# Performance work log

Hardware: AMD Instinct MI355X
Metric: run time of the kernel (lower is better)

## Reference

```python
import jax, jax.numpy as jnp
import numpy as np

B, T, C, H = 4, 2048, 768, 12
D = C // H  # head dim = 64

def setup_inputs() -> dict:
    key = jax.random.key(0)
    k1, k2, k3, k4, k5 = jax.random.split(key, 5)
    s = 0.02
    x = jax.random.normal(k1, (B, T, C), dtype=jnp.float32)
    w_qkv = jax.random.normal(k2, (3 * C, C), dtype=jnp.float32) * s  # torch Linear weight [out,in]
    b_qkv = jax.random.normal(k3, (3 * C,), dtype=jnp.float32) * s
    w_proj = jax.random.normal(k4, (C, C), dtype=jnp.float32) * s
    b_proj = jax.random.normal(k5, (C,), dtype=jnp.float32) * s
    return {"x": x, "w_qkv": w_qkv, "b_qkv": b_qkv, "w_proj": w_proj, "b_proj": b_proj}

def reference(x, w_qkv, b_qkv, w_proj, b_proj):
    Bx, Tx, Cx = x.shape
    # qkv projection: torch Linear y = x @ W.T + b
    qkv = x @ w_qkv.T + b_qkv                      # [B,T,3C]
    qkv = qkv.reshape(Bx, Tx, 3, H, D)
    q, k, v = qkv[:, :, 0], qkv[:, :, 1], qkv[:, :, 2]  # each [B,T,H,D]
    scale = 1.0 / jnp.sqrt(jnp.float32(D))
    scores = jnp.einsum('bqhd,bkhd->bhqk', q, k) * scale  # [B,H,T,T]
    causal = jnp.tril(jnp.ones((Tx, Tx), dtype=bool))
    scores = jnp.where(causal[None, None], scores, -jnp.inf)
    attn = jax.nn.softmax(scores, axis=-1)
    out = jnp.einsum('bhqk,bkhd->bqhd', attn, v).reshape(Bx, Tx, Cx)
    return out @ w_proj.T + b_proj
```

## Files before the change

kernel.cpp:

```cpp
#include <hip/hip_runtime.h>
#include <hip/hip_bf16.h>
#include <cstdint>
#include <cstddef>

typedef __bf16 bf16_t;
typedef __bf16 bf16x8 __attribute__((ext_vector_type(8)));
typedef __bf16 bf16x4 __attribute__((ext_vector_type(4)));
typedef float f32x4 __attribute__((ext_vector_type(4)));
typedef float f32x16 __attribute__((ext_vector_type(16)));

constexpr int B_ = 4, T_ = 2048, C_ = 768, H_ = 12, D_ = 64;
constexpr size_t QKV_ELEMS = (size_t)B_ * H_ * T_ * D_;
constexpr size_t AO_ELEMS  = (size_t)B_ * T_ * C_;
constexpr size_t WPB_ELEMS = (size_t)C_ * C_;

__device__ __forceinline__ void gload16(const bf16_t* g, bf16_t* l) {
    __builtin_amdgcn_global_load_lds(
        (const __attribute__((address_space(1))) unsigned int*)g,
        (__attribute__((address_space(3))) unsigned int*)l, 16, 0, 0);
}

__global__ __launch_bounds__(256)
void conv_bf16_3(const float* __restrict__ a, bf16_t* __restrict__ oa, int na8,
                 const float* __restrict__ b, bf16_t* __restrict__ ob, int nb8,
                 const float* __restrict__ c, bf16_t* __restrict__ oc, int nc8)
{
    int i = blockIdx.x * 256 + threadIdx.x;
    if (i >= na8 + nb8 + nc8) return;
    const float* src; bf16_t* dst; int idx;
    if (i < na8)             { src = a; dst = oa; idx = i; }
    else if (i < na8 + nb8)  { src = b; dst = ob; idx = i - na8; }
    else                     { src = c; dst = oc; idx = i - na8 - nb8; }
    const float4* p = reinterpret_cast<const float4*>(src + (size_t)idx * 8);
    float4 f0 = p[0], f1 = p[1];
    bf16x8 t;
    t[0]=(bf16_t)f0.x; t[1]=(bf16_t)f0.y; t[2]=(bf16_t)f0.z; t[3]=(bf16_t)f0.w;
    t[4]=(bf16_t)f1.x; t[5]=(bf16_t)f1.y; t[6]=(bf16_t)f1.z; t[7]=(bf16_t)f1.w;
    *reinterpret_cast<bf16x8*>(dst + (size_t)idx * 8) = t;
}

__global__ __launch_bounds__(256, 3)
void qkv_gemm(const bf16_t* __restrict__ xb, const bf16_t* __restrict__ wb,
              const float* __restrict__ bias,
              bf16_t* __restrict__ q, bf16_t* __restrict__ k, bf16_t* __restrict__ v)
{
    __shared__ alignas(16) bf16_t As[128 * 64];
    __shared__ alignas(16) bf16_t Bs[128 * 64];
    const int tid  = threadIdx.x;
    const int lane = tid & 63;
    const int w    = tid >> 6;
    const int wm = w >> 1, wn = w & 1;
    const int bm = blockIdx.x & 63;
    const int bn = blockIdx.x >> 6;
    const int m0 = bm * 128, n0 = bn * 128;
    const int lcol = lane & 15, lgrp = lane >> 4;
    const int srow = lane >> 3;
    const int scol = ((lane & 7) ^ srow) * 8;

    const bf16_t* ag = xb + (size_t)(m0 + w * 32 + srow) * C_ + scol;
    const bf16_t* bg = wb + (size_t)(n0 + w * 32 + srow) * C_ + scol;
    bf16_t* al = &As[(w * 32) * 64];
    bf16_t* bl = &Bs[(w * 32) * 64];

    f32x4 acc[4][4] = {};

    for (int kt = 0; kt < C_; kt += 64) {
        __syncthreads();
        #pragma unroll
        for (int p = 0; p < 4; ++p) {
            gload16(ag + (size_t)(p * 8) * C_ + kt, al + p * 8 * 64);
            gload16(bg + (size_t)(p * 8) * C_ + kt, bl + p * 8 * 64);
        }
        __syncthreads();
        #pragma unroll
        for (int kk = 0; kk < 2; ++kk) {
            bf16x8 af[4], bfr[4];
            #pragma unroll
            for (int i = 0; i < 4; ++i) {
                const int R = wm * 64 + i * 16 + lcol;
                af[i] = *reinterpret_cast<const bf16x8*>(&As[R * 64 + (((kk*4 + lgrp) ^ (R & 7)) << 3)]);
            }
            #pragma unroll
            for (int j = 0; j < 4; ++j) {
                const int R = wn * 64 + j * 16 + lcol;
                bfr[j] = *reinterpret_cast<const bf16x8*>(&Bs[R * 64 + (((kk*4 + lgrp) ^ (R & 7)) << 3)]);
            }
            #pragma unroll
            for (int i = 0; i < 4; ++i)
                #pragma unroll
                for (int j = 0; j < 4; ++j)
                    acc[i][j] = __builtin_amdgcn_mfma_f32_16x16x32_bf16(af[i], bfr[j], acc[i][j], 0, 0, 0);
        }
    }

    #pragma unroll
    for (int j = 0; j < 4; ++j) {
        const int n = n0 + wn * 64 + j * 16 + lcol;
        const float bv = bias[n];
        const int s = n / C_, rem = n % C_;
        const int h = rem >> 6, d = rem & 63;
        bf16_t* dst = (s == 0) ? q : (s == 1) ? k : v;
        #pragma unroll
        for (int i = 0; i < 4; ++i) {
            #pragma unroll
            for (int r = 0; r < 4; ++r) {
                const int m = m0 + wm * 64 + i * 16 + lgrp * 4 + r;
                const int b = m >> 11, t = m & (T_ - 1);
                dst[(((size_t)(b * H_ + h)) * T_ + t) * D_ + d] = (bf16_t)(acc[i][j][r] + bv);
            }
        }
    }
}

__global__ __launch_bounds__(256, 3)
void attn_fwd(const bf16_t* __restrict__ qg, const bf16_t* __restrict__ kg,
              const bf16_t* __restrict__ vg, bf16_t* __restrict__ og)
{
    __shared__ alignas(16) bf16_t lds[4 * 64 * 64];
    bf16_t* Ks = lds;
    bf16_t* Vt = lds + 2 * 64 * 64;
    float*  scr = (float*)lds;

    const int tid  = threadIdx.x;
    const int lane = tid & 63;
    const int w    = tid >> 6;
    const int wq   = w >> 1;
    const int ws   = w & 1;
    const int l31  = lane & 31;
    const int hi   = lane >> 5;
    const int qi   = blockIdx.x / 48;
    const int bh   = blockIdx.x % 48;
    const int qt   = 31 - qi;
    const int q0   = qt * 64;
    const int qw   = q0 + wq * 32;
    const size_t base = (size_t)bh * T_ * D_;
    const int qrow = qw + l31;

    const float SCL = 0.125f * 1.44269504f;
    bf16x8 bq[4];
    #pragma unroll
    for (int kt = 0; kt < 4; ++kt) {
        bf16x8 t = *reinterpret_cast<const bf16x8*>(qg + base + (size_t)qrow * D_ + kt*16 + hi*8);
        #pragma unroll
        for (int e = 0; e < 8; ++e) t[e] = (bf16_t)((float)t[e] * SCL);
        bq[kt] = t;
    }

    f32x16 ot0 = {};
    f32x16 ot1 = {};
    float m = -1e30f, rowl = 0.0f;

    const int sgr = tid & 7;
    union U8 { bf16x8 v; uint32_t u[4]; };
    union UP { uint32_t u[4]; bf16x8 v; };

    const int ntiles = qt + 1;
    const int np = (ntiles + 1) >> 1;

    for (int p = 0; p < np; ++p) {
        __syncthreads();
        #pragma unroll
        for (int par = 0; par < 2; ++par) {
            const int t = 2 * p + par;
            if (t >= ntiles) break;
            const size_t toff = (size_t)t * 64 * D_;
            #pragma unroll
            for (int pp = 0; pp < 2; ++pp) {
                const int g = pp * 256 + tid;
                const int key = g >> 3, slot = g & 7;
                bf16x8 kv = *reinterpret_cast<const bf16x8*>(
                    kg + base + toff + (size_t)key * D_ + slot * 8);
                *reinterpret_cast<bf16x8*>(
                    Ks + par * 4096 + key * 64 + ((slot ^ (key & 7)) << 3)) = kv;
            }
            {
                const int va = tid >> 3;
                U8 v0, v1;
                v0.v = *reinterpret_cast<const bf16x8*>(
                    vg + base + toff + (size_t)(2 * va) * D_ + sgr * 8);
                v1.v = *reinterpret_cast<const bf16x8*>(
                    vg + base + toff + (size_t)(2 * va + 1) * D_ + sgr * 8);
                #pragma unroll
                for (int j = 0; j < 8; ++j) {
                    const int d = sgr * 8 + j;
                    const int ss = ((va >> 2) ^ j ^ sgr) & 7;
                    uint32_t wd = __builtin_amdgcn_perm(v1.u[j >> 1], v0.u[j >> 1],
                                                        (j & 1) ? 0x07060302u : 0x05040100u);
                    *reinterpret_cast<uint32_t*>(
                        Vt + par * 4096 + d * 64 + ss * 8 + (va & 3) * 2) = wd;
                }
            }
        }
        __syncthreads();

        const int t = 2 * p + ws;
        if (t >= ntiles) continue;
        const bf16_t* Kb = Ks + ws * 4096;
        const bf16_t* Vb = Vt + ws * 4096;
        const int kv0 = t * 64;

        #pragma unroll
        for (int sk = 0; sk < 2; ++sk) {
            const int kvs = kv0 + sk * 32;
            if (sk == 1 && kvs > qw + 31) continue;

            f32x16 s = {};
            __builtin_amdgcn_s_setprio(1);
            #pragma unroll
            for (int kt = 0; kt < 4; ++kt) {
                const int keyl = sk * 32 + l31;
                const int slot = kt * 2 + hi;
                bf16x8 ka = *reinterpret_cast<const bf16x8*>(
                    Kb + keyl * 64 + ((slot ^ (keyl & 7)) << 3));
                s = __builtin_amdgcn_mfma_f32_32x32x16_bf16(ka, bq[kt], s, 0, 0, 0);
            }
            __builtin_amdgcn_s_setprio(0);
            if (kvs + 31 > qw) {
                #pragma unroll
                for (int r = 0; r < 16; ++r) {
                    const int key = kvs + (r & 3) + 8 * (r >> 2) + 4 * hi;
                    if (key > qrow) s[r] = -1e30f;
                }
            }
            float a0 = fmaxf(fmaxf(s[0],  s[1]),  s[2]);
            float a1 = fmaxf(fmaxf(s[3],  s[4]),  s[5]);
            float a2 = fmaxf(fmaxf(s[6],  s[7]),  s[8]);
            float a3 = fmaxf(fmaxf(s[9],  s[10]), s[11]);
            float a4 = fmaxf(fmaxf(s[12], s[13]), s[14]);
            float b0 = fmaxf(fmaxf(a0, a1), a2);
            float b1 = fmaxf(fmaxf(a3, a4), s[15]);
            float mt = fmaxf(b0, b1);
            mt = fmaxf(mt, __shfl_xor(mt, 32));
            if (!__all(mt <= m + 8.0f)) {
                const float mnew = fmaxf(m, mt);
                const float alpha = exp2f(m - mnew);
                #pragma unroll
                for (int r = 0; r < 16; ++r) { ot0[r] *= alpha; ot1[r] *= alpha; }
                rowl *= alpha;
                m = mnew;
            }
            #pragma unroll
            for (int r = 0; r < 16; ++r) s[r] = exp2f(s[r] - m);
            float t0 = (s[0]+s[1]) + (s[2]+s[3]);
            float t1 = (s[4]+s[5]) + (s[6]+s[7]);
            float t2 = (s[8]+s[9]) + (s[10]+s[11]);
            float t3 = (s[12]+s[13]) + (s[14]+s[15]);
            float rs = (t0 + t1) + (t2 + t3);
            rs += __shfl_xor(rs, 32);
            rowl += rs;

            uint32_t c0, c1, c2, c3, c4, c5, c6, c7;
            asm("v_cvt_pk_bf16_f32 %0, %1, %2" : "=v"(c0) : "v"(s[0]),  "v"(s[1]));
            asm("v_cvt_pk_bf16_f32 %0, %1, %2" : "=v"(c1) : "v"(s[2]),  "v"(s[3]));
            asm("v_cvt_pk_bf16_f32 %0, %1, %2" : "=v"(c2) : "v"(s[4]),  "v"(s[5]));
            asm("v_cvt_pk_bf16_f32 %0, %1, %2" : "=v"(c3) : "v"(s[6]),  "v"(s[7]));
            asm("v_cvt_pk_bf16_f32 %0, %1, %2" : "=v"(c4) : "v"(s[8]),  "v"(s[9]));
            asm("v_cvt_pk_bf16_f32 %0, %1, %2" : "=v"(c5) : "v"(s[10]), "v"(s[11]));
            asm("v_cvt_pk_bf16_f32 %0, %1, %2" : "=v"(c6) : "v"(s[12]), "v"(s[13]));
            asm("v_cvt_pk_bf16_f32 %0, %1, %2" : "=v"(c7) : "v"(s[14]), "v"(s[15]));
            asm("v_permlane32_swap_b32 %0, %1" : "+v"(c0), "+v"(c2));
            asm("v_permlane32_swap_b32 %0, %1" : "+v"(c1), "+v"(c3));
            asm("v_permlane32_swap_b32 %0, %1" : "+v"(c4), "+v"(c6));
            asm("v_permlane32_swap_b32 %0, %1" : "+v"(c5), "+v"(c7));
            UP pa0; pa0.u[0] = c0; pa0.u[1] = c1; pa0.u[2] = c2; pa0.u[3] = c3;
            UP pa1; pa1.u[0] = c4; pa1.u[1] = c5; pa1.u[2] = c6; pa1.u[3] = c7;

            __builtin_amdgcn_s_setprio(1);
            #pragma unroll
            for (int dblk = 0; dblk < 2; ++dblk) {
                const int d = dblk * 32 + l31;
                f32x16& o = dblk ? ot1 : ot0;
                #pragma unroll
                for (int ktile = 0; ktile < 2; ++ktile) {
                    const int kslot = sk * 4 + ktile * 2 + hi;
                    const int ss = kslot ^ (d & 7) ^ ((d >> 3) & 7);
                    bf16x8 va = *reinterpret_cast<const bf16x8*>(Vb + d * 64 + (ss << 3));
                    o = __builtin_amdgcn_mfma_f32_32x32x16_bf16(va, ktile ? pa1.v : pa0.v, o, 0, 0, 0);
                }
            }
            __builtin_amdgcn_s_setprio(0);
        }
    }

    __syncthreads();
    if (ws == 1) {
        float* s = scr + (wq * 64 + lane) * 35;
        #pragma unroll
        for (int r = 0; r < 16; ++r) { s[r] = ot0[r]; s[16 + r] = ot1[r]; }
        s[32] = m; s[33] = rowl;
    }
    __syncthreads();
    if (ws == 0) {
        const float* s = scr + (wq * 64 + lane) * 35;
        const float m1 = s[32], l1 = s[33];
        const float mn = fmaxf(m, m1);
        const float f0 = exp2f(m - mn);
        const float f1 = exp2f(m1 - mn);
        const float linv = 1.0f / (rowl * f0 + l1 * f1);
        const int b = bh / H_, h = bh % H_;
        bf16_t* dst = &og[((size_t)b * T_ + qrow) * C_ + h * D_];
        #pragma unroll
        for (int dblk = 0; dblk < 2; ++dblk) {
            const f32x16& o = dblk ? ot1 : ot0;
            #pragma unroll
            for (int qd = 0; qd < 4; ++qd) {
                bf16x4 v4;
                #pragma unroll
                for (int r = 0; r < 4; ++r) {
                    const float ov = o[qd * 4 + r] * f0 + s[dblk * 16 + qd * 4 + r] * f1;
                    v4[r] = (bf16_t)(ov * linv);
                }
                *reinterpret_cast<bf16x4*>(dst + dblk * 32 + qd * 8 + hi * 4) = v4;
            }
        }
    }
}

__global__ __launch_bounds__(256, 3)
void proj_gemm(const bf16_t* __restrict__ ao, const bf16_t* __restrict__ wpb,
               const float* __restrict__ bias, float* __restrict__ out)
{
    __shared__ alignas(16) bf16_t As[128 * 64];
    __shared__ alignas(16) bf16_t Bs[128 * 64];
    const int tid  = threadIdx.x;
    const int lane = tid & 63;
    const int w    = tid >> 6;
    const int wm = w >> 1, wn = w & 1;
    const int bm = blockIdx.x & 63;
    const int bn = blockIdx.x >> 6;
    const int m0 = bm * 128, n0 = bn * 128;
    const int lcol = lane & 15, lgrp = lane >> 4;
    const int srow = lane >> 3;
    const int scol = ((lane & 7) ^ srow) * 8;

    const bf16_t* ag = ao  + (size_t)(m0 + w * 32 + srow) * C_ + scol;
    const bf16_t* bg = wpb + (size_t)(n0 + w * 32 + srow) * C_ + scol;
    bf16_t* al = &As[(w * 32) * 64];
    bf16_t* bl = &Bs[(w * 32) * 64];

    f32x4 acc[4][4] = {};

    for (int kt = 0; kt < C_; kt += 64) {
        __syncthreads();
        #pragma unroll
        for (int p = 0; p < 4; ++p) {
            gload16(ag + (size_t)(p * 8) * C_ + kt, al + p * 8 * 64);
            gload16(bg + (size_t)(p * 8) * C_ + kt, bl + p * 8 * 64);
        }
        __syncthreads();
        #pragma unroll
        for (int kk = 0; kk < 2; ++kk) {
            bf16x8 af[4], bfr[4];
            #pragma unroll
            for (int i = 0; i < 4; ++i) {
                const int R = wm * 64 + i * 16 + lcol;
                af[i] = *reinterpret_cast<const bf16x8*>(&As[R * 64 + (((kk*4 + lgrp) ^ (R & 7)) << 3)]);
            }
            #pragma unroll
            for (int j = 0; j < 4; ++j) {
                const int R = wn * 64 + j * 16 + lcol;
                bfr[j] = *reinterpret_cast<const bf16x8*>(&Bs[R * 64 + (((kk*4 + lgrp) ^ (R & 7)) << 3)]);
            }
            #pragma unroll
            for (int i = 0; i < 4; ++i)
                #pragma unroll
                for (int j = 0; j < 4; ++j)
                    acc[i][j] = __builtin_amdgcn_mfma_f32_16x16x32_bf16(af[i], bfr[j], acc[i][j], 0, 0, 0);
        }
    }

    #pragma unroll
    for (int j = 0; j < 4; ++j) {
        const int n = n0 + wn * 64 + j * 16 + lcol;
        const float bv = bias[n];
        #pragma unroll
        for (int i = 0; i < 4; ++i) {
            #pragma unroll
            for (int r = 0; r < 4; ++r) {
                const int m = m0 + wm * 64 + i * 16 + lgrp * 4 + r;
                out[(size_t)m * C_ + n] = acc[i][j][r] + bv;
            }
        }
    }
}

extern "C" void kernel_launch(void* const* d_in, const int* in_sizes, int n_in,
                              void* d_out, int out_size, void* d_ws, size_t ws_size,
                              hipStream_t stream)
{
    const float* x      = (const float*)d_in[0];
    const float* w_qkv  = (const float*)d_in[1];
    const float* b_qkv  = (const float*)d_in[2];
    const float* w_proj = (const float*)d_in[3];
    const float* b_proj = (const float*)d_in[4];
    float* out = (float*)d_out;

    bf16_t* ws = (bf16_t*)d_ws;
    bf16_t* q   = ws;
    bf16_t* k   = ws +     QKV_ELEMS;
    bf16_t* v   = ws + 2 * QKV_ELEMS;
    bf16_t* ao  = ws + 3 * QKV_ELEMS;
    bf16_t* xb  = ao;
    bf16_t* wqb = (bf16_t*)d_out;

    const size_t need = (3 * QKV_ELEMS + AO_ELEMS + WPB_ELEMS) * sizeof(bf16_t);
    if (ws_size >= need) {
        bf16_t* wpb = ws + 3 * QKV_ELEMS + AO_ELEMS;
        conv_bf16_3<<<dim3(4224), 256, 0, stream>>>(
            x, xb, 786432, w_qkv, wqb, 221184, w_proj, wpb, 73728);
        qkv_gemm<<<dim3(64 * 18), 256, 0, stream>>>(xb, wqb, b_qkv, q, k, v);
        attn_fwd<<<dim3(32 * 48), 256, 0, stream>>>(q, k, v, ao);
        proj_gemm<<<dim3(64 * 6), 256, 0, stream>>>(ao, wpb, b_proj, out);
    } else {
        bf16_t* wpb = k;
        conv_bf16_3<<<dim3(3936), 256, 0, stream>>>(
            x, xb, 786432, w_qkv, wqb, 221184, (const float*)nullptr, (bf16_t*)nullptr, 0);
        qkv_gemm<<<dim3(64 * 18), 256, 0, stream>>>(xb, wqb, b_qkv, q, k, v);
        attn_fwd<<<dim3(32 * 48), 256, 0, stream>>>(q, k, v, ao);
        conv_bf16_3<<<dim3(288), 256, 0, stream>>>(
            w_proj, wpb, 73728, (const float*)nullptr, (bf16_t*)nullptr, 0,
            (const float*)nullptr, (bf16_t*)nullptr, 0);
        proj_gemm<<<dim3(64 * 6), 256, 0, stream>>>(ao, wpb, b_proj, out);
    }
}
```

Baseline: 119.0 us.

## Double attention query tile to 128 rows with 512-thread blocks sharing K/V

The attention kernel now uses 512-thread blocks that each cover 128 query rows instead of 64. Each staged pair of K/V tiles in LDS is shared by twice as many query warps, halving global K/V loads per query row and halving the grid size. In exchange there are fewer, larger blocks, coarser causal imbalance, and the LDS scratch grows (18432 elements). The hidden epilogue must also be consistent with 4 query-warp groups and the larger scratch area.

Result: no change. 119.1 us (+0.1%).

```diff
diff --git a/kernel.cpp b/kernel.cpp
--- a/kernel.cpp
+++ b/kernel.cpp
@@ -112,11 +112,11 @@
     }
 }
 
-__global__ __launch_bounds__(256, 3)
+__global__ __launch_bounds__(512, 4)
 void attn_fwd(const bf16_t* __restrict__ qg, const bf16_t* __restrict__ kg,
               const bf16_t* __restrict__ vg, bf16_t* __restrict__ og)
 {
-    __shared__ alignas(16) bf16_t lds[4 * 64 * 64];
+    __shared__ alignas(16) bf16_t lds[18432];
     bf16_t* Ks = lds;
     bf16_t* Vt = lds + 2 * 64 * 64;
     float*  scr = (float*)lds;
@@ -130,8 +130,8 @@
     const int hi   = lane >> 5;
     const int qi   = blockIdx.x / 48;
     const int bh   = blockIdx.x % 48;
-    const int qt   = 31 - qi;
-    const int q0   = qt * 64;
+    const int qt   = 15 - qi;
+    const int q0   = qt * 128;
     const int qw   = q0 + wq * 32;
     const size_t base = (size_t)bh * T_ * D_;
     const int qrow = qw + l31;
@@ -150,54 +150,48 @@
     f32x16 ot1 = {};
     float m = -1e30f, rowl = 0.0f;
 
-    const int sgr = tid & 7;
     union U8 { bf16x8 v; uint32_t u[4]; };
     union UP { uint32_t u[4]; bf16x8 v; };
 
-    const int ntiles = qt + 1;
-    const int np = (ntiles + 1) >> 1;
+    const int np = qt + 1;
 
     for (int p = 0; p < np; ++p) {
         __syncthreads();
         #pragma unroll
-        for (int par = 0; par < 2; ++par) {
-            const int t = 2 * p + par;
-            if (t >= ntiles) break;
-            const size_t toff = (size_t)t * 64 * D_;
-            #pragma unroll
-            for (int pp = 0; pp < 2; ++pp) {
-                const int g = pp * 256 + tid;
-                const int key = g >> 3, slot = g & 7;
-                bf16x8 kv = *reinterpret_cast<const bf16x8*>(
-                    kg + base + toff + (size_t)key * D_ + slot * 8);
-                *reinterpret_cast<bf16x8*>(
-                    Ks + par * 4096 + key * 64 + ((slot ^ (key & 7)) << 3)) = kv;
-            }
-            {
-                const int va = tid >> 3;
-                U8 v0, v1;
-                v0.v = *reinterpret_cast<const bf16x8*>(
-                    vg + base + toff + (size_t)(2 * va) * D_ + sgr * 8);
-                v1.v = *reinterpret_cast<const bf16x8*>(
-                    vg + base + toff + (size_t)(2 * va + 1) * D_ + sgr * 8);
-                #pragma unroll
-                for (int j = 0; j < 8; ++j) {
-                    const int d = sgr * 8 + j;
-                    const int ss = ((va >> 2) ^ j ^ sgr) & 7;
-                    uint32_t wd = __builtin_amdgcn_perm(v1.u[j >> 1], v0.u[j >> 1],
-                                                        (j & 1) ? 0x07060302u : 0x05040100u);
-                    *reinterpret_cast<uint32_t*>(
-                        Vt + par * 4096 + d * 64 + ss * 8 + (va & 3) * 2) = wd;
-                }
-            }
-        }
-        __syncthreads();
-
-        const int t = 2 * p + ws;
-        if (t >= ntiles) continue;
+        for (int pp = 0; pp < 2; ++pp) {
+            const int g = pp * 512 + tid;
+            const int par = g >> 9, key = (g >> 3) & 63, slot = g & 7;
+            bf16x8 kv = *reinterpret_cast<const bf16x8*>(
+                kg + base + (size_t)(2 * p + par) * 64 * D_ + (size_t)key * D_ + slot * 8);
+            *reinterpret_cast<bf16x8*>(
+                Ks + par * 4096 + key * 64 + ((slot ^ (key & 7)) << 3)) = kv;
+        }
+        {
+            const int par = tid >> 8;
+            const int va  = (tid >> 3) & 31;
+            const int sg  = tid & 7;
+            const size_t toff = (size_t)(2 * p + par) * 64 * D_;
+            U8 v0, v1;
+            v0.v = *reinterpret_cast<const bf16x8*>(
+                vg + base + toff + (size_t)(2 * va) * D_ + sg * 8);
+            v1.v = *reinterpret_cast<const bf16x8*>(
+                vg + base + toff + (size_t)(2 * va + 1) * D_ + sg * 8);
+            #pragma unroll
+            for (int j = 0; j < 8; ++j) {
+                const int d = sg * 8 + j;
+                const int ss = ((va >> 2) ^ j ^ sg) & 7;
+                uint32_t wd = __builtin_amdgcn_perm(v1.u[j >> 1], v0.u[j >> 1],
+                                                    (j & 1) ? 0x07060302u : 0x05040100u);
+                *reinterpret_cast<uint32_t*>(
+                    Vt + par * 4096 + d * 64 + ss * 8 + (va & 3) * 2) = wd;
+            }
+        }
+        __syncthreads();
+
+        const int kv0 = (2 * p + ws) * 64;
+        if (kv0 > qw + 31) continue;
         const bf16_t* Kb = Ks + ws * 4096;
         const bf16_t* Vb = Vt + ws * 4096;
-        const int kv0 = t * 64;
 
         #pragma unroll
         for (int sk = 0; sk < 2; ++sk) {
@@ -409,14 +403,14 @@
         conv_bf16_3<<<dim3(4224), 256, 0, stream>>>(
             x, xb, 786432, w_qkv, wqb, 221184, w_proj, wpb, 73728);
         qkv_gemm<<<dim3(64 * 18), 256, 0, stream>>>(xb, wqb, b_qkv, q, k, v);
-        attn_fwd<<<dim3(32 * 48), 256, 0, stream>>>(q, k, v, ao);
+        attn_fwd<<<dim3(16 * 48), 512, 0, stream>>>(q, k, v, ao);
         proj_gemm<<<dim3(64 * 6), 256, 0, stream>>>(ao, wpb, b_proj, out);
     } else {
         bf16_t* wpb = k;
         conv_bf16_3<<<dim3(3936), 256, 0, stream>>>(
             x, xb, 786432, w_qkv, wqb, 221184, (const float*)nullptr, (bf16_t*)nullptr, 0);
         qkv_gemm<<<dim3(64 * 18), 256, 0, stream>>>(xb, wqb, b_qkv, q, k, v);
-        attn_fwd<<<dim3(32 * 48), 256, 0, stream>>>(q, k, v, ao);
+        attn_fwd<<<dim3(16 * 48), 512, 0, stream>>>(q, k, v, ao);
         conv_bf16_3<<<dim3(288), 256, 0, stream>>>(
             w_proj, wpb, 73728, (const float*)nullptr, (bf16_t*)nullptr, 0,
             (const float*)nullptr, (bf16_t*)nullptr, 0);
```
